# Kernel tuning notes

Measured on AMD Instinct MI355X. Metric: run time of the kernel, lower is better.

The kernel has to match this reference:

```python
import jax, jax.numpy as jnp
import numpy as np


def mha_col0(x0, w_in, b_in, w_out, b_out):
    # x0: [N, D]. torch MHA (1 head, batch_first=False): seq dim = N, this is the
    # batch-0 slice (the only one consumed by tmp[:, 0]).
    qkv = x0 @ w_in.T + b_in                     # [N, 3D]
    q, k, v = jnp.split(qkv, 3, axis=-1)         # each [N, D]
    scale = 1.0 / np.sqrt(np.float32(q.shape[-1]))
    attn = jax.nn.softmax((q * scale) @ k.T, axis=-1)   # [N, N]
    return (attn @ v) @ w_out.T + b_out          # [N, D]


def sage(x_src, x_dst, ei, w_l, b_l, w_r):
    # PyG SAGEConv with aggr='sum': out = lin_l(sum_j x_src[src_j]) + lin_r(x_dst)
    msg = x_src[ei[0]]                                            # [E, D] gather
    agg = jax.ops.segment_sum(msg, ei[1], num_segments=x_dst.shape[0])  # [Nd, D] scatter
    return agg @ w_l.T + b_l + x_dst @ w_r.T


def setup_inputs() -> dict:
    key = jax.random.key(0)
    ks = jax.random.split(key, 24)
    N, C, D, E = 8192, 6, 128, 262144
    s = 0.05
    p = lambda k, shape: jax.random.normal(k, shape, dtype=jnp.float32) * s
    return {
        "x_A": jax.random.normal(ks[0], (N, C, D), dtype=jnp.float32),
        "x_B": jax.random.normal(ks[1], (N, C, D), dtype=jnp.float32),
        "ei_AB": jax.random.randint(ks[2], (2, E), 0, N),
        "ei_BA": jax.random.randint(ks[3], (2, E), 0, N),
        "ei_AA": jax.random.randint(ks[4], (2, E), 0, N),
        "inW_A": p(ks[5], (3 * D, D)), "inB_A": p(ks[6], (3 * D,)),
        "outW_A": p(ks[7], (D, D)), "outB_A": p(ks[8], (D,)),
        "inW_B": p(ks[9], (3 * D, D)), "inB_B": p(ks[10], (3 * D,)),
        "outW_B": p(ks[11], (D, D)), "outB_B": p(ks[12], (D,)),
        "wl_AB": p(ks[13], (D, D)), "bl_AB": p(ks[14], (D,)), "wr_AB": p(ks[15], (D, D)),
        "wl_BA": p(ks[16], (D, D)), "bl_BA": p(ks[17], (D,)), "wr_BA": p(ks[18], (D, D)),
        "wl_AA": p(ks[19], (D, D)), "bl_AA": p(ks[20], (D,)), "wr_AA": p(ks[21], (D, D)),
    }


def reference(x_A, x_B, ei_AB, ei_BA, ei_AA,
              inW_A, inB_A, outW_A, outB_A,
              inW_B, inB_B, outW_B, outB_B,
              wl_AB, bl_AB, wr_AB,
              wl_BA, bl_BA, wr_BA,
              wl_AA, bl_AA, wr_AA):
    # per-type attention, keeping only column 0 (tmp[:, 0])
    h_A = mha_col0(x_A[:, 0], inW_A, inB_A, outW_A, outB_A)   # [N, D]
    h_B = mha_col0(x_B[:, 0], inW_B, inB_B, outW_B, outB_B)   # [N, D]
    # HeteroConv(aggr='sum'): B gets A->B; A gets B->A + A->A
    out_B = sage(h_A, h_B, ei_AB, wl_AB, bl_AB, wr_AB)
    out_A = (sage(h_B, h_A, ei_BA, wl_BA, bl_BA, wr_BA)
             + sage(h_A, h_A, ei_AA, wl_AA, bl_AA, wr_AA))
    # re-attach remaining column tokens (x is 3D)
    new_A = jnp.concatenate((out_A[:, None, :], x_A[:, 1:]), axis=1)  # [N, C, D]
    new_B = jnp.concatenate((out_B[:, None, :], x_B[:, 1:]), axis=1)
    return new_A, new_B
```

## Files before the change

kernel.cpp:

```cpp
#include <hip/hip_runtime.h>
#include <hip/hip_bf16.h>

typedef unsigned short u16;
typedef unsigned int u32;
typedef __attribute__((ext_vector_type(8))) short bf16x8;
typedef __attribute__((ext_vector_type(4))) short bf16x4;
typedef __attribute__((ext_vector_type(4))) float f32x4;
typedef __attribute__((ext_vector_type(16))) float f32x16;

#define MFMA(a,b,c)   __builtin_amdgcn_mfma_f32_16x16x32_bf16((a),(b),(c),0,0,0)
#define MFMA32(a,b,c) __builtin_amdgcn_mfma_f32_32x32x16_bf16((a),(b),(c),0,0,0)

__device__ __forceinline__ float bf2f(u16 u){
  union { float f; u32 i; } c; c.i = ((u32)u) << 16; return c.f;
}
__device__ __forceinline__ u16 f2bf(float f){
  __hip_bfloat16 h = __float2bfloat16(f);
  u16 u; __builtin_memcpy(&u, &h, 2); return u;
}
__device__ __forceinline__ bf16x8 ld8f(const float* p){
  bf16x8 r;
  #pragma unroll
  for (int i = 0; i < 8; i++) r[i] = (short)f2bf(p[i]);
  return r;
}
__device__ __forceinline__ u32 cvtpk(float a, float b){
  u32 r; asm volatile("v_cvt_pk_bf16_f32 %0, %1, %2" : "=v"(r) : "v"(a), "v"(b)); return r;
}
__device__ __forceinline__ void pl32swap(u32 &a, u32 &b){
  asm volatile("v_permlane32_swap_b32 %0, %1" : "+v"(a), "+v"(b));
}

#define QSCALE 0.12751741528681559f

struct WPrepArgs { const float* src[10]; int off[10]; int total4; };
__global__ __launch_bounds__(256) void prelude_kernel(
    WPrepArgs a, u16* __restrict__ wdst,
    const int* __restrict__ e0, const int* __restrict__ e1, const int* __restrict__ e2,
    int* __restrict__ cnt,
    const float* __restrict__ xA, float* __restrict__ outA,
    const float* __restrict__ xB, float* __restrict__ outB,
    int Nn, int E, int W, int HB, int TB)
{
  const int tid = threadIdx.x;
  int b = blockIdx.x;
  if (b < W) {
    int i = b * 256 + tid;
    if (i >= a.total4) return;
    int e = i * 4;
    int j = 0;
    #pragma unroll
    for (int k = 1; k < 10; k++) if (e >= a.off[k]) j = k;
    f32x4 v = *(const f32x4*)(a.src[j] + (e - a.off[j]));
    bf16x4 o;
    #pragma unroll
    for (int r = 0; r < 4; r++) o[r] = (short)f2bf(v[r]);
    *(bf16x4*)(wdst + e) = o;
    return;
  }
  b -= W;
  if (b < 3 * HB) {
    int t = b / HB;
    int e = (b % HB) * 256 + tid;
    if (e >= E) return;
    const int* ei = t == 0 ? e0 : (t == 1 ? e1 : e2);
    atomicAdd(&cnt[t * Nn + ei[E + e]], 1);
    return;
  }
  b -= 3 * HB;
  {
    int t = b / TB;
    int idx = (b % TB) * 256 + tid;
    if (idx >= Nn * 160) return;
    const float* x = t ? xB : xA;
    float* o = t ? outB : outA;
    int n = idx / 160, r = idx % 160;
    size_t off = (size_t)n * 768 + 128 + (size_t)r * 4;
    *(f32x4*)(o + off) = *(const f32x4*)(x + off);
  }
}

__global__ __launch_bounds__(256) void qkv_scan_kernel(
    const float* __restrict__ xA, const u16* __restrict__ wA, const float* __restrict__ bA, u16* __restrict__ yA,
    const float* __restrict__ xB, const u16* __restrict__ wB, const float* __restrict__ bB, u16* __restrict__ yB,
    u16* __restrict__ vtA_, u16* __restrict__ vtB_,
    const int* __restrict__ cnt, int* __restrict__ off, int* __restrict__ work,
    int Nn, int N, int LB)
{
  const int tid = threadIdx.x;
  int b = blockIdx.x;
  if (b >= 2 * LB) {
    const int t = b - 2 * LB;
    const int* c = cnt + t * Nn;
    int* o = off + t * (Nn + 1);
    int* w = work + t * Nn;
    __shared__ int part[256];
    const int base = tid * 32;
    int loc[32], s = 0;
    #pragma unroll
    for (int i = 0; i < 32; i++) { loc[i] = s; s += c[base + i]; }
    part[tid] = s;
    __syncthreads();
    #pragma unroll
    for (int st = 1; st < 256; st <<= 1) {
      int v = (tid >= st) ? part[tid - st] : 0;
      __syncthreads();
      part[tid] += v;
      __syncthreads();
    }
    int pre = (tid == 0) ? 0 : part[tid - 1];
    #pragma unroll
    for (int i = 0; i < 32; i++) { int p = pre + loc[i]; o[base + i] = p; w[base + i] = p; }
    if (tid == 255) o[Nn] = part[255];
    return;
  }
  const int yb = b & 1, xb = b >> 1;
  const float* x = yb ? xB : xA;
  const u16* w = yb ? wB : wA;
  const float* bb = yb ? bB : bA;
  u16* y = yb ? yB : yA;
  u16* vt = yb ? vtB_ : vtA_;
  const int lane = tid & 63, wid = tid >> 6;
  const int g = lane >> 4, l15 = lane & 15;
  const int row0 = xb * 64 + wid * 16;

  bf16x8 a[4];
  const float* xr = x + (size_t)(row0 + l15) * 768;
  #pragma unroll
  for (int kk = 0; kk < 4; kk++) a[kk] = ld8f(xr + kk * 32 + g * 8);

  const f32x4 fz = {0.f, 0.f, 0.f, 0.f};
  for (int j0 = 0; j0 < 384; j0 += 16) {
    f32x4 acc = fz;
    const u16* wr_ = w + (size_t)(j0 + l15) * 128;
    #pragma unroll
    for (int kk = 0; kk < 4; kk++)
      acc = MFMA(a[kk], *(const bf16x8*)(wr_ + kk * 32 + g * 8), acc);
    float bv = bb[j0 + l15];
    if (j0 < 128) {
      #pragma unroll
      for (int r = 0; r < 4; r++)
        y[(size_t)(row0 + g * 4 + r) * 256 + j0 + l15] = f2bf((acc[r] + bv) * QSCALE);
    } else if (j0 < 256) {
      #pragma unroll
      for (int r = 0; r < 4; r++)
        y[(size_t)(row0 + g * 4 + r) * 256 + j0 + l15] = f2bf(acc[r] + bv);
    } else {
      bf16x4 o4;
      #pragma unroll
      for (int r = 0; r < 4; r++) o4[r] = (short)f2bf(acc[r] + bv);
      *(bf16x4*)(vt + (size_t)(j0 - 256 + l15) * N + row0 + g * 4) = o4;
    }
  }
}

__global__ __launch_bounds__(256, 2) void flash_sort_kernel(
    const u16* __restrict__ qkvA, const u16* __restrict__ vtA,
    const u16* __restrict__ qkvB, const u16* __restrict__ vtB,
    u16* __restrict__ part_acc, float* __restrict__ part_l,
    const int* __restrict__ e0, const int* __restrict__ e1, const int* __restrict__ e2,
    int* __restrict__ work, int* __restrict__ ssrc,
    int N, int segsz, int SEG, int NB128, int FB, int HB, int E)
{
  __shared__ __align__(16) u16 Kt[2][64 * 128];
  __shared__ __align__(16) u16 Vtt[2][128 * 64];
  const int tid = threadIdx.x;
  int b = blockIdx.x;
  if (b >= FB) {
    int sb = b - FB;
    int t = sb / HB;
    int e = (sb % HB) * 256 + tid;
    if (e >= E) return;
    const int* ei = t == 0 ? e0 : (t == 1 ? e1 : e2);
    int s = ei[e], d = ei[E + e];
    int pos = atomicAdd(&work[t * N + d], 1);
    ssrc[(size_t)t * E + pos] = s;
    return;
  }
  const int x = b % NB128;
  const int rest = b / NB128;
  const int seg = rest % SEG;
  const int ty = rest / SEG;
  const u16* qkv = ty ? qkvB : qkvA;
  const u16* vt  = ty ? vtB  : vtA;
  const int lane = tid & 63, wid = tid >> 6;
  const int l31 = lane & 31, h = lane >> 5, l7 = lane & 7;
  const int q = x * 128 + wid * 32 + l31;
  const int kvbase = seg * segsz;

  int rk[4], ck[4], cks[4], rv[4], cv[4], cvs[4];
  #pragma unroll
  for (int i = 0; i < 4; i++) {
    int ch = tid + i * 256;
    rk[i] = ch >> 4; ck[i] = (ch & 15) * 8; cks[i] = ck[i] ^ ((rk[i] & 7) << 3);
    rv[i] = ch >> 3; cv[i] = (ch & 7) * 8;  cvs[i] = cv[i] ^ ((rv[i] & 7) << 3);
  }

  bf16x8 aQ[8];
  const u16* qr = qkv + (size_t)q * 256;
  #pragma unroll
  for (int kk = 0; kk < 8; kk++) aQ[kk] = *(const bf16x8*)(qr + kk * 16 + h * 8);

  f32x16 accO[4];
  #pragma unroll
  for (int d = 0; d < 4; d++) accO[d] = (f32x16)0.f;
  float l_ = 0.f;

  {
    #pragma unroll
    for (int i = 0; i < 4; i++) {
      bf16x8 kv8 = *(const bf16x8*)(qkv + 128 + (size_t)(kvbase + rk[i]) * 256 + ck[i]);
      bf16x8 vv8 = *(const bf16x8*)(vt + (size_t)rv[i] * N + kvbase + cv[i]);
      *(bf16x8*)&Kt[0][rk[i] * 128 + cks[i]] = kv8;
      *(bf16x8*)&Vtt[0][rv[i] * 64 + cvs[i]] = vv8;
    }
  }
  __syncthreads();

  int cur = 0;
  for (int kt = 0; kt < segsz; kt += 64) {
    const bool pfch = (kt + 64 < segsz);
    bf16x8 kreg[4], vreg[4];
    if (pfch) {
      const int kv0n = kvbase + kt + 64;
      #pragma unroll
      for (int i = 0; i < 4; i++) {
        kreg[i] = *(const bf16x8*)(qkv + 128 + (size_t)(kv0n + rk[i]) * 256 + ck[i]);
        vreg[i] = *(const bf16x8*)(vt + (size_t)rv[i] * N + kv0n + cv[i]);
      }
    }

    const u16* KtC = Kt[cur];
    const u16* VtC = Vtt[cur];

    f32x16 sc0 = (f32x16)0.f, sc1 = (f32x16)0.f;
    #pragma unroll
    for (int kk = 0; kk < 8; kk++) {
      const int co = ((kk * 2 + h) * 8) ^ (l7 << 3);
      bf16x8 aK0 = *(bf16x8*)&KtC[l31 * 128 + co];
      bf16x8 aK1 = *(bf16x8*)&KtC[(32 + l31) * 128 + co];
      sc0 = MFMA32(aK0, aQ[kk], sc0);
      sc1 = MFMA32(aK1, aQ[kk], sc1);
    }

    #pragma unroll
    for (int i = 0; i < 16; i++) {
      float e0 = __builtin_exp2f(sc0[i]);
      float e1 = __builtin_exp2f(sc1[i]);
      sc0[i] = e0; sc1[i] = e1; l_ += e0 + e1;
    }

    #pragma unroll
    for (int t = 0; t < 4; t++) {
      const f32x16& s_ = (t < 2) ? sc0 : sc1;
      const int jA = (t & 1) * 2, jB = jA + 1;
      u32 a0 = cvtpk(s_[jA * 4 + 0], s_[jA * 4 + 1]);
      u32 b0 = cvtpk(s_[jB * 4 + 0], s_[jB * 4 + 1]);
      u32 a1 = cvtpk(s_[jA * 4 + 2], s_[jA * 4 + 3]);
      u32 b1 = cvtpk(s_[jB * 4 + 2], s_[jB * 4 + 3]);
      pl32swap(a0, b0); pl32swap(a1, b1);
      union { u32 w[4]; bf16x8 v; } pf;
      pf.w[0] = a0; pf.w[1] = a1; pf.w[2] = b0; pf.w[3] = b1;
      #pragma unroll
      for (int db = 0; db < 4; db++) {
        bf16x8 aV = *(bf16x8*)&VtC[(db * 32 + l31) * 64 + (((t * 2 + h) * 8) ^ (l7 << 3))];
        accO[db] = MFMA32(aV, pf.v, accO[db]);
      }
    }

    if (pfch) {
      const int nb = cur ^ 1;
      #pragma unroll
      for (int i = 0; i < 4; i++) {
        *(bf16x8*)&Kt[nb][rk[i] * 128 + cks[i]] = kreg[i];
        *(bf16x8*)&Vtt[nb][rv[i] * 64 + cvs[i]] = vreg[i];
      }
    }
    __syncthreads();
    cur ^= 1;
  }

  l_ += __shfl_xor(l_, 32);

  const size_t pbase = ((size_t)(ty * SEG + seg) * N + q) * 128;
  #pragma unroll
  for (int d = 0; d < 4; d++)
    #pragma unroll
    for (int j = 0; j < 4; j++) {
      bf16x4 o4;
      #pragma unroll
      for (int r = 0; r < 4; r++) o4[r] = (short)f2bf(accO[d][j * 4 + r]);
      *(bf16x4*)(part_acc + pbase + d * 32 + j * 8 + h * 4) = o4;
    }
  if (h == 0)
    part_l[(size_t)(ty * SEG + seg) * N + q] = l_;
}

__global__ __launch_bounds__(256) void combine_hproj_kernel(
    const u16* __restrict__ part_acc, const float* __restrict__ part_l,
    const u16* __restrict__ woutA, const float* __restrict__ boutA, u16* __restrict__ hA,
    const u16* __restrict__ woutB, const float* __restrict__ boutB, u16* __restrict__ hB,
    int N, int SEG)
{
  __shared__ __align__(16) u16 ot[64 * 136];
  const int t = blockIdx.y;
  const u16* w = t ? woutB : woutA;
  const float* bb = t ? boutB : boutA;
  u16* hOut = t ? hB : hA;
  const int tid = threadIdx.x;
  const int row = tid >> 2, qt = tid & 3;
  const int grow = blockIdx.x * 64 + row;

  float l = 0.f;
  for (int s = 0; s < SEG; s++)
    l += part_l[(size_t)(t * SEG + s) * N + grow];
  float acc[32];
  #pragma unroll
  for (int i = 0; i < 32; i++) acc[i] = 0.f;
  for (int s = 0; s < SEG; s++) {
    const u16* pa = part_acc + ((size_t)(t * SEG + s) * N + grow) * 128 + qt * 32;
    #pragma unroll
    for (int j = 0; j < 4; j++) {
      bf16x8 vch = *(const bf16x8*)(pa + j * 8);
      #pragma unroll
      for (int i = 0; i < 8; i++) acc[j * 8 + i] += bf2f((u16)vch[i]);
    }
  }
  const float inv = 1.f / l;
  #pragma unroll
  for (int j = 0; j < 4; j++) {
    bf16x8 oc;
    #pragma unroll
    for (int i = 0; i < 8; i++) oc[i] = (short)f2bf(acc[j * 8 + i] * inv);
    *(bf16x8*)&ot[row * 136 + qt * 32 + j * 8] = oc;
  }
  __syncthreads();

  const int lane = tid & 63, wid = tid >> 6;
  const int g = lane >> 4, l15 = lane & 15;
  const int row0 = wid * 16;
  bf16x8 a[4];
  #pragma unroll
  for (int kk = 0; kk < 4; kk++) a[kk] = *(bf16x8*)&ot[(row0 + l15) * 136 + kk * 32 + g * 8];
  const f32x4 fz = {0.f, 0.f, 0.f, 0.f};
  for (int j0 = 0; j0 < 128; j0 += 16) {
    f32x4 acc2 = fz;
    const u16* wr_ = w + (size_t)(j0 + l15) * 128;
    #pragma unroll
    for (int kk = 0; kk < 4; kk++)
      acc2 = MFMA(a[kk], *(const bf16x8*)(wr_ + kk * 32 + g * 8), acc2);
    float bv = bb[j0 + l15];
    #pragma unroll
    for (int r = 0; r < 4; r++)
      hOut[(size_t)(blockIdx.x * 64 + row0 + g * 4 + r) * 128 + j0 + l15] = f2bf(acc2[r] + bv);
  }
}

__global__ __launch_bounds__(256) void aggregate_kernel(
    const u16* __restrict__ h0, const u16* __restrict__ h1, const u16* __restrict__ h2,
    const int* __restrict__ off, const int* __restrict__ ssrc,
    u16* __restrict__ agg, int Nn, int E)
{
  const int t = blockIdx.y;
  const u16* h = t == 0 ? h0 : (t == 1 ? h1 : h2);
  const int* o = off + t * (Nn + 1);
  const int* ss = ssrc + (size_t)t * E;
  u16* a = agg + (size_t)t * Nn * 128;
  const int wid = threadIdx.x >> 6, lane = threadIdx.x & 63;
  const int d = blockIdx.x * 4 + wid;
  const int s0 = o[d], s1 = o[d + 1];
  float a0 = 0.f, a1 = 0.f;
  int e = s0;
  for (; e + 3 < s1; e += 4) {
    int r0 = ss[e], r1 = ss[e + 1], r2 = ss[e + 2], r3 = ss[e + 3];
    u32 v0 = *(const u32*)(h + (size_t)r0 * 128 + lane * 2);
    u32 v1 = *(const u32*)(h + (size_t)r1 * 128 + lane * 2);
    u32 v2 = *(const u32*)(h + (size_t)r2 * 128 + lane * 2);
    u32 v3 = *(const u32*)(h + (size_t)r3 * 128 + lane * 2);
    a0 += bf2f((u16)(v0 & 0xffff)) + bf2f((u16)(v1 & 0xffff)) + bf2f((u16)(v2 & 0xffff)) + bf2f((u16)(v3 & 0xffff));
    a1 += bf2f((u16)(v0 >> 16)) + bf2f((u16)(v1 >> 16)) + bf2f((u16)(v2 >> 16)) + bf2f((u16)(v3 >> 16));
  }
  for (; e < s1; e++) {
    u32 v = *(const u32*)(h + (size_t)ss[e] * 128 + lane * 2);
    a0 += bf2f((u16)(v & 0xffff));
    a1 += bf2f((u16)(v >> 16));
  }
  *(u32*)(a + (size_t)d * 128 + lane * 2) = cvtpk(a0, a1);
}

__global__ __launch_bounds__(256) void sage_out_kernel(
    const u16* __restrict__ aggAB, const u16* __restrict__ wlAB, const float* __restrict__ blAB,
    const u16* __restrict__ hB, const u16* __restrict__ wrAB,
    const u16* __restrict__ aggBA, const u16* __restrict__ wlBA, const float* __restrict__ blBA,
    const u16* __restrict__ hA, const u16* __restrict__ wrBA,
    const u16* __restrict__ aggAA, const u16* __restrict__ wlAA, const float* __restrict__ blAA,
    const u16* __restrict__ wrAA,
    float* __restrict__ outA, float* __restrict__ outB)
{
  const bool two = (blockIdx.y == 1);
  const u16* agg1 = two ? aggBA : aggAB;
  const u16* wl1  = two ? wlBA  : wlAB;
  const float* bl1 = two ? blBA : blAB;
  const u16* h1   = two ? hA : hB;
  const u16* wr1  = two ? wrBA : wrAB;
  float* out = two ? outA : outB;

  const int lane = threadIdx.x & 63, wid = threadIdx.x >> 6;
  const int g = lane >> 4, l15 = lane & 15;
  const int row0 = blockIdx.x * 64 + wid * 16;

  bf16x8 a1[4], aH1[4], a2[4];
  const u16* ar1 = agg1 + (size_t)(row0 + l15) * 128;
  const u16* hr1 = h1 + (size_t)(row0 + l15) * 128;
  #pragma unroll
  for (int kk = 0; kk < 4; kk++) {
    a1[kk] = *(const bf16x8*)(ar1 + kk * 32 + g * 8);
    aH1[kk] = *(const bf16x8*)(hr1 + kk * 32 + g * 8);
  }
  if (two) {
    const u16* ar2 = aggAA + (size_t)(row0 + l15) * 128;
    #pragma unroll
    for (int kk = 0; kk < 4; kk++)
      a2[kk] = *(const bf16x8*)(ar2 + kk * 32 + g * 8);
  }

  const f32x4 fz = {0.f, 0.f, 0.f, 0.f};
  for (int j0 = 0; j0 < 128; j0 += 16) {
    f32x4 acc = fz;
    const u16* w1 = wl1 + (size_t)(j0 + l15) * 128;
    const u16* w2 = wr1 + (size_t)(j0 + l15) * 128;
    #pragma unroll
    for (int kk = 0; kk < 4; kk++) {
      acc = MFMA(a1[kk], *(const bf16x8*)(w1 + kk * 32 + g * 8), acc);
      acc = MFMA(aH1[kk], *(const bf16x8*)(w2 + kk * 32 + g * 8), acc);
    }
    float bias = bl1[j0 + l15];
    if (two) {
      const u16* w3 = wlAA + (size_t)(j0 + l15) * 128;
      const u16* w4 = wrAA + (size_t)(j0 + l15) * 128;
      #pragma unroll
      for (int kk = 0; kk < 4; kk++) {
        acc = MFMA(a2[kk], *(const bf16x8*)(w3 + kk * 32 + g * 8), acc);
        acc = MFMA(aH1[kk], *(const bf16x8*)(w4 + kk * 32 + g * 8), acc);
      }
      bias += blAA[j0 + l15];
    }
    #pragma unroll
    for (int r = 0; r < 4; r++)
      out[(size_t)(row0 + g * 4 + r) * 768 + j0 + l15] = acc[r] + bias;
  }
}

extern "C" void kernel_launch(void* const* d_in, const int* in_sizes, int n_in,
                              void* d_out, int out_size, void* d_ws, size_t ws_size,
                              hipStream_t stream)
{
  const int D = 128, C = 6;
  const int N = in_sizes[0] / (C * D);
  const int E = in_sizes[2] / 2;

  const float* xA = (const float*)d_in[0];
  const float* xB = (const float*)d_in[1];
  const int* eiAB = (const int*)d_in[2];
  const int* eiBA = (const int*)d_in[3];
  const int* eiAA = (const int*)d_in[4];
  const float* inW_A  = (const float*)d_in[5];
  const float* inB_A  = (const float*)d_in[6];
  const float* outW_A = (const float*)d_in[7];
  const float* outB_A = (const float*)d_in[8];
  const float* inW_B  = (const float*)d_in[9];
  const float* inB_B  = (const float*)d_in[10];
  const float* outW_B = (const float*)d_in[11];
  const float* outB_B = (const float*)d_in[12];
  const float* wlAB = (const float*)d_in[13];
  const float* blAB = (const float*)d_in[14];
  const float* wrAB = (const float*)d_in[15];
  const float* wlBA = (const float*)d_in[16];
  const float* blBA = (const float*)d_in[17];
  const float* wrBA = (const float*)d_in[18];
  const float* wlAA = (const float*)d_in[19];
  const float* blAA = (const float*)d_in[20];
  const float* wrAA = (const float*)d_in[21];

  u16* qkvA = (u16*)d_ws;
  u16* qkvB = qkvA + (size_t)N * 256;
  u16* vtA  = qkvB + (size_t)N * 256;
  u16* vtB  = vtA + (size_t)D * N;
  u16* hA   = vtB + (size_t)D * N;
  u16* hB   = hA + (size_t)N * D;
  u16* wbf  = hB + (size_t)N * D;
  const int wsz[10] = {3*D*D, 3*D*D, D*D, D*D, D*D, D*D, D*D, D*D, D*D, D*D};
  const float* wsrc[10] = {inW_A, inW_B, outW_A, outW_B, wlAB, wrAB, wlBA, wrBA, wlAA, wrAA};
  WPrepArgs wp; int wtot = 0;
  for (int k = 0; k < 10; k++) { wp.src[k] = wsrc[k]; wp.off[k] = wtot; wtot += wsz[k]; }
  wp.total4 = wtot / 4;
  u16* w_inA  = wbf + wp.off[0];
  u16* w_inB  = wbf + wp.off[1];
  u16* w_outA = wbf + wp.off[2];
  u16* w_outB = wbf + wp.off[3];
  u16* w_wlAB = wbf + wp.off[4];
  u16* w_wrAB = wbf + wp.off[5];
  u16* w_wlBA = wbf + wp.off[6];
  u16* w_wrBA = wbf + wp.off[7];
  u16* w_wlAA = wbf + wp.off[8];
  u16* w_wrAA = wbf + wp.off[9];

  int* cnt  = (int*)(wbf + wtot);
  int* off  = cnt + 3 * N;
  int* work = off + 3 * (N + 1);
  int* ssrc = work + 3 * N;
  char* uni = (char*)(ssrc + 3 * E);
  size_t base_b = (size_t)(uni - (char*)d_ws);
  size_t agg_b = (size_t)3 * N * 128 * 2;
  auto part_b = [&](int S){ return (size_t)2 * S * N * 128 * 2 + (size_t)2 * S * N * 4; };
  int SEG = 4;
  while (SEG > 1 && ws_size < base_b + (part_b(SEG) > agg_b ? part_b(SEG) : agg_b)) SEG >>= 1;
  const int segsz = N / SEG;
  u16* part_acc = (u16*)uni;
  float* part_l = (float*)(part_acc + (size_t)2 * SEG * N * 128);
  u16* aggAB = (u16*)uni;
  u16* aggBA = aggAB + (size_t)N * D;
  u16* aggAA = aggBA + (size_t)N * D;

  float* outA = (float*)d_out;
  float* outB = outA + (size_t)N * C * D;

  dim3 blk(256);
  const int W = (wp.total4 + 255) / 256;
  const int HB = (E + 255) / 256;
  const int TB = (N * 160 + 255) / 256;
  const int LB = N / 64;
  const int NB128 = N / 128;
  const int FB = NB128 * SEG * 2;
  (void)hipMemsetAsync(cnt, 0, (size_t)3 * N * sizeof(int), stream);
  prelude_kernel<<<dim3(W + 3 * HB + 2 * TB), blk, 0, stream>>>(
      wp, wbf, eiAB, eiBA, eiAA, cnt, xA, outA, xB, outB, N, E, W, HB, TB);
  qkv_scan_kernel<<<dim3(2 * LB + 3), blk, 0, stream>>>(
      xA, w_inA, inB_A, qkvA, xB, w_inB, inB_B, qkvB, vtA, vtB,
      cnt, off, work, N, N, LB);
  flash_sort_kernel<<<dim3(FB + 3 * HB), blk, 0, stream>>>(
      qkvA, vtA, qkvB, vtB, part_acc, part_l,
      eiAB, eiBA, eiAA, work, ssrc, N, segsz, SEG, NB128, FB, HB, E);
  combine_hproj_kernel<<<dim3(N / 64, 2), blk, 0, stream>>>(part_acc, part_l,
                                                            w_outA, outB_A, hA,
                                                            w_outB, outB_B, hB, N, SEG);
  aggregate_kernel<<<dim3(N / 4, 3), blk, 0, stream>>>(hA, hB, hA, off, ssrc, aggAB, N, E);
  sage_out_kernel<<<dim3(N / 64, 2), blk, 0, stream>>>(
      aggAB, w_wlAB, blAB, hB, w_wrAB,
      aggBA, w_wlBA, blBA, hA, w_wrBA,
      aggAA, w_wlAA, blAA, w_wrAA, outA, outB);
}
```

Baseline: 229.1 us.

## Halve flash attention KV tile to 32 rows, raise occupancy, double KV segments

Shrinks the attention kernel's KV tile from 64 to 32 keys per iteration. This halves the shared-memory K/V double buffers and the score registers, and re-lays out the V tile so 128 d-rows fit a 64-column swizzled layout. Launch bounds are raised to 3 blocks per CU and the KV split count goes from 4 to 8 segments to expose more parallel blocks. In exchange there are twice as many loop iterations and barriers, less work per MFMA batch, and more partial results to write and merge.

```diff
diff --git a/kernel.cpp b/kernel.cpp
--- a/kernel.cpp
+++ b/kernel.cpp
@@ -154,7 +154,7 @@
   }
 }
 
-__global__ __launch_bounds__(256, 2) void flash_sort_kernel(
+__global__ __launch_bounds__(256, 3) void flash_sort_kernel(
     const u16* __restrict__ qkvA, const u16* __restrict__ vtA,
     const u16* __restrict__ qkvB, const u16* __restrict__ vtB,
     u16* __restrict__ part_acc, float* __restrict__ part_l,
@@ -162,8 +162,8 @@
     int* __restrict__ work, int* __restrict__ ssrc,
     int N, int segsz, int SEG, int NB128, int FB, int HB, int E)
 {
-  __shared__ __align__(16) u16 Kt[2][64 * 128];
-  __shared__ __align__(16) u16 Vtt[2][128 * 64];
+  __shared__ __align__(16) u16 Kt[2][32 * 128];
+  __shared__ __align__(16) u16 Vtt[2][64 * 64];
   const int tid = threadIdx.x;
   int b = blockIdx.x;
   if (b >= FB) {
@@ -188,12 +188,15 @@
   const int q = x * 128 + wid * 32 + l31;
   const int kvbase = seg * segsz;
 
-  int rk[4], ck[4], cks[4], rv[4], cv[4], cvs[4];
-  #pragma unroll
-  for (int i = 0; i < 4; i++) {
+  int rk[2], ck[2], cks[2], vd[2], vc[2], vidx[2];
+  #pragma unroll
+  for (int i = 0; i < 2; i++) {
     int ch = tid + i * 256;
     rk[i] = ch >> 4; ck[i] = (ch & 15) * 8; cks[i] = ck[i] ^ ((rk[i] & 7) << 3);
-    rv[i] = ch >> 3; cv[i] = (ch & 7) * 8;  cvs[i] = cv[i] ^ ((rv[i] & 7) << 3);
+    int d = ch >> 2, c8 = (ch & 3) * 8;
+    vd[i] = d; vc[i] = c8;
+    int row = d & 63, col = (c8 + ((d >> 6) << 5)) ^ ((row & 7) << 3);
+    vidx[i] = row * 64 + col;
   }
 
   bf16x8 aQ[8];
@@ -208,62 +211,59 @@
 
   {
     #pragma unroll
-    for (int i = 0; i < 4; i++) {
+    for (int i = 0; i < 2; i++) {
       bf16x8 kv8 = *(const bf16x8*)(qkv + 128 + (size_t)(kvbase + rk[i]) * 256 + ck[i]);
-      bf16x8 vv8 = *(const bf16x8*)(vt + (size_t)rv[i] * N + kvbase + cv[i]);
+      bf16x8 vv8 = *(const bf16x8*)(vt + (size_t)vd[i] * N + kvbase + vc[i]);
       *(bf16x8*)&Kt[0][rk[i] * 128 + cks[i]] = kv8;
-      *(bf16x8*)&Vtt[0][rv[i] * 64 + cvs[i]] = vv8;
+      *(bf16x8*)&Vtt[0][vidx[i]] = vv8;
     }
   }
   __syncthreads();
 
   int cur = 0;
-  for (int kt = 0; kt < segsz; kt += 64) {
-    const bool pfch = (kt + 64 < segsz);
-    bf16x8 kreg[4], vreg[4];
+  for (int kt = 0; kt < segsz; kt += 32) {
+    const bool pfch = (kt + 32 < segsz);
+    bf16x8 kreg[2], vreg[2];
     if (pfch) {
-      const int kv0n = kvbase + kt + 64;
-      #pragma unroll
-      for (int i = 0; i < 4; i++) {
+      const int kv0n = kvbase + kt + 32;
+      #pragma unroll
+      for (int i = 0; i < 2; i++) {
         kreg[i] = *(const bf16x8*)(qkv + 128 + (size_t)(kv0n + rk[i]) * 256 + ck[i]);
-        vreg[i] = *(const bf16x8*)(vt + (size_t)rv[i] * N + kv0n + cv[i]);
+        vreg[i] = *(const bf16x8*)(vt + (size_t)vd[i] * N + kv0n + vc[i]);
       }
     }
 
     const u16* KtC = Kt[cur];
     const u16* VtC = Vtt[cur];
 
-    f32x16 sc0 = (f32x16)0.f, sc1 = (f32x16)0.f;
+    f32x16 sc = (f32x16)0.f;
     #pragma unroll
     for (int kk = 0; kk < 8; kk++) {
-      const int co = ((kk * 2 + h) * 8) ^ (l7 << 3);
-      bf16x8 aK0 = *(bf16x8*)&KtC[l31 * 128 + co];
-      bf16x8 aK1 = *(bf16x8*)&KtC[(32 + l31) * 128 + co];
-      sc0 = MFMA32(aK0, aQ[kk], sc0);
-      sc1 = MFMA32(aK1, aQ[kk], sc1);
+      bf16x8 aK = *(bf16x8*)&KtC[l31 * 128 + (((kk * 2 + h) * 8) ^ (l7 << 3))];
+      sc = MFMA32(aK, aQ[kk], sc);
     }
 
     #pragma unroll
     for (int i = 0; i < 16; i++) {
-      float e0 = __builtin_exp2f(sc0[i]);
-      float e1 = __builtin_exp2f(sc1[i]);
-      sc0[i] = e0; sc1[i] = e1; l_ += e0 + e1;
-    }
-
-    #pragma unroll
-    for (int t = 0; t < 4; t++) {
-      const f32x16& s_ = (t < 2) ? sc0 : sc1;
-      const int jA = (t & 1) * 2, jB = jA + 1;
-      u32 a0 = cvtpk(s_[jA * 4 + 0], s_[jA * 4 + 1]);
-      u32 b0 = cvtpk(s_[jB * 4 + 0], s_[jB * 4 + 1]);
-      u32 a1 = cvtpk(s_[jA * 4 + 2], s_[jA * 4 + 3]);
-      u32 b1 = cvtpk(s_[jB * 4 + 2], s_[jB * 4 + 3]);
+      float e = __builtin_exp2f(sc[i]);
+      sc[i] = e; l_ += e;
+    }
+
+    #pragma unroll
+    for (int t = 0; t < 2; t++) {
+      const int jA = t * 2, jB = t * 2 + 1;
+      u32 a0 = cvtpk(sc[jA * 4 + 0], sc[jA * 4 + 1]);
+      u32 b0 = cvtpk(sc[jB * 4 + 0], sc[jB * 4 + 1]);
+      u32 a1 = cvtpk(sc[jA * 4 + 2], sc[jA * 4 + 3]);
+      u32 b1 = cvtpk(sc[jB * 4 + 2], sc[jB * 4 + 3]);
       pl32swap(a0, b0); pl32swap(a1, b1);
       union { u32 w[4]; bf16x8 v; } pf;
       pf.w[0] = a0; pf.w[1] = a1; pf.w[2] = b0; pf.w[3] = b1;
       #pragma unroll
       for (int db = 0; db < 4; db++) {
-        bf16x8 aV = *(bf16x8*)&VtC[(db * 32 + l31) * 64 + (((t * 2 + h) * 8) ^ (l7 << 3))];
+        const int row = (db & 1) * 32 + l31;
+        const int col = (t * 16 + h * 8 + ((db >> 1) << 5)) ^ (l7 << 3);
+        bf16x8 aV = *(bf16x8*)&VtC[row * 64 + col];
         accO[db] = MFMA32(aV, pf.v, accO[db]);
       }
     }
@@ -271,9 +271,9 @@
     if (pfch) {
       const int nb = cur ^ 1;
       #pragma unroll
-      for (int i = 0; i < 4; i++) {
+      for (int i = 0; i < 2; i++) {
         *(bf16x8*)&Kt[nb][rk[i] * 128 + cks[i]] = kreg[i];
-        *(bf16x8*)&Vtt[nb][rv[i] * 64 + cvs[i]] = vreg[i];
+        *(bf16x8*)&Vtt[nb][vidx[i]] = vreg[i];
       }
     }
     __syncthreads();
@@ -513,7 +513,7 @@
   size_t base_b = (size_t)(uni - (char*)d_ws);
   size_t agg_b = (size_t)3 * N * 128 * 2;
   auto part_b = [&](int S){ return (size_t)2 * S * N * 128 * 2 + (size_t)2 * S * N * 4; };
-  int SEG = 4;
+  int SEG = 8;
   while (SEG > 1 && ws_size < base_b + (part_b(SEG) > agg_b ? part_b(SEG) : agg_b)) SEG >>= 1;
   const int segsz = N / SEG;
   u16* part_acc = (u16*)uni;
```

New measurement: 246.6 us. +7.6%, slower.
